# Performance work log

Measured on AMD Instinct MI355X. Metric: run time of the kernel, lower is better.

The kernel has to match this reference:

```python
import jax, jax.numpy as jnp
import numpy as np

N_NODES = 100000
N_EDGES = 1600000
IN_CH = 128
HID = 128
OUT_CH = 40


def setup_inputs() -> dict:
    key = jax.random.key(0)
    ks = jax.random.split(key, 8)
    x = jax.random.normal(ks[0], (N_NODES, IN_CH), dtype=jnp.float32)
    edge_index = jax.random.randint(ks[1], (2, N_EDGES), 0, N_NODES, dtype=jnp.int64)
    s1 = 1.0 / np.sqrt(IN_CH)
    s2 = 1.0 / np.sqrt(HID)
    # SAGEConv layer 1: lin_l (applied to aggregated neighbors, has bias), lin_r (applied to root, no bias)
    Wl1 = jax.random.uniform(ks[2], (IN_CH, HID), jnp.float32, -s1, s1)
    b1 = jnp.zeros((HID,), jnp.float32)
    Wr1 = jax.random.uniform(ks[3], (IN_CH, HID), jnp.float32, -s1, s1)
    # SAGEConv layer 2
    Wl2 = jax.random.uniform(ks[4], (HID, OUT_CH), jnp.float32, -s2, s2)
    b2 = jnp.zeros((OUT_CH,), jnp.float32)
    Wr2 = jax.random.uniform(ks[5], (HID, OUT_CH), jnp.float32, -s2, s2)
    return {"x": x, "edge_index": edge_index, "Wl1": Wl1, "b1": b1, "Wr1": Wr1,
            "Wl2": Wl2, "b2": b2, "Wr2": Wr2}


def _sage_conv(x, src, dst, Wl, b, Wr):
    # mean-aggregate source-node features onto target nodes (PyG SAGEConv, aggr='mean')
    msg_sum = jax.ops.segment_sum(x[src], dst, num_segments=N_NODES)  # [N, F]
    deg = jax.ops.segment_sum(jnp.ones((src.shape[0],), x.dtype), dst, num_segments=N_NODES)
    aggr = msg_sum / jnp.maximum(deg, 1.0)[:, None]
    return aggr @ Wl + b + x @ Wr


def reference(x, edge_index, Wl1, b1, Wr1, Wl2, b2, Wr2):
    src, dst = edge_index[0], edge_index[1]
    h = _sage_conv(x, src, dst, Wl1, b1, Wr1)
    h = jax.nn.relu(h)  # dropout is identity in eval mode
    h = _sage_conv(h, src, dst, Wl2, b2, Wr2)
    return jax.nn.log_softmax(h, axis=-1)
```

## Files before the change

### kernel.cpp

```cpp
#include <hip/hip_runtime.h>
#include <math.h>

#define NN 100000
#define NE 1600000
#define NBUK ((NN + 255) / 256)
#define CAP 5120
#define NBLK_A 500
#define EPB (NE / NBLK_A)
#define GPB (EPB / 4)
#define MT ((NN + 127) / 128)
#define MPAD ((size_t)MT * 128)

typedef __attribute__((ext_vector_type(8))) short short8;
typedef __attribute__((ext_vector_type(4))) float f32x4;
typedef __attribute__((ext_vector_type(4))) int i32x4;
typedef unsigned short ushort_t;
typedef unsigned int uint_t;

__device__ inline ushort_t f2bf(float f) {
    uint_t u = __builtin_bit_cast(uint_t, f);
    u += 0x7FFFu + ((u >> 16) & 1u);
    return (ushort_t)(u >> 16);
}
__device__ inline float bits2f(uint_t u) { return __builtin_bit_cast(float, u); }
__device__ inline float lo16(uint_t u) { return bits2f(u << 16); }
__device__ inline float hi16(uint_t u) { return bits2f(u & 0xFFFF0000u); }

__device__ inline void gload_lds16(const void* g, void* l) {
    __builtin_amdgcn_global_load_lds(
        (const __attribute__((address_space(1))) unsigned int*)g,
        (__attribute__((address_space(3))) unsigned int*)l, 16, 0, 0);
}

__global__ __launch_bounds__(256) void cvt_bf16(const float* __restrict__ x,
                                                ushort_t* __restrict__ xb) {
    const int total = NN * 128 / 8;
    const f32x4* src = (const f32x4*)x;
    for (int g = blockIdx.x * 256 + threadIdx.x; g < total; g += gridDim.x * 256) {
        f32x4 v0 = __builtin_nontemporal_load(src + (size_t)g * 2);
        f32x4 v1 = __builtin_nontemporal_load(src + (size_t)g * 2 + 1);
        i32x4 o;
        o[0] = ((uint_t)f2bf(v0[1]) << 16) | (uint_t)f2bf(v0[0]);
        o[1] = ((uint_t)f2bf(v0[3]) << 16) | (uint_t)f2bf(v0[2]);
        o[2] = ((uint_t)f2bf(v1[1]) << 16) | (uint_t)f2bf(v1[0]);
        o[3] = ((uint_t)f2bf(v1[3]) << 16) | (uint_t)f2bf(v1[2]);
        *(i32x4*)(xb + (size_t)g * 8) = o;
    }
}

__global__ void pack_weights(const float* __restrict__ Wl1, const float* __restrict__ Wr1,
                             const float* __restrict__ Wl2, const float* __restrict__ Wr2,
                             ushort_t* __restrict__ W1T, ushort_t* __restrict__ W2T) {
    int gid = blockIdx.x * blockDim.x + threadIdx.x;
    if (gid < 256 * 128) {
        int n = gid >> 7, k = gid & 127;
        float v = (n < 128) ? Wl1[k * 128 + n] : Wr1[k * 128 + (n - 128)];
        W1T[gid] = f2bf(v);
    } else {
        int g = gid - 256 * 128;
        if (g < 128 * 128) {
            int n = g >> 7, k = g & 127;
            float v = 0.0f;
            if (n < 40)      v = Wl2[k * 40 + n];
            else if (n < 80) v = Wr2[k * 40 + (n - 40)];
            W2T[g] = f2bf(v);
        }
    }
}

__global__ __launch_bounds__(256) void hist_buckets(const int* __restrict__ ei,
                                                    int* __restrict__ bhist) {
    __shared__ int h[NBUK];
    int tid = threadIdx.x;
    for (int i = tid; i < NBUK; i += 256) h[i] = 0;
    __syncthreads();
    const i32x4* dsts = (const i32x4*)(ei + NE + blockIdx.x * EPB);
    for (int g = tid; g < GPB; g += 256) {
        i32x4 d = __builtin_nontemporal_load(dsts + g);
#pragma unroll
        for (int j = 0; j < 4; ++j) atomicAdd(&h[d[j] >> 8], 1);
    }
    __syncthreads();
    for (int i = tid; i < NBUK; i += 256)
        if (h[i]) atomicAdd(&bhist[i], h[i]);
}

__global__ __launch_bounds__(512) void scan_buckets(const int* __restrict__ bhist,
                                                    int* __restrict__ boff,
                                                    int* __restrict__ gcur,
                                                    int* __restrict__ offsets) {
    __shared__ int part[512];
    int t = threadIdx.x;
    int v = (t < NBUK) ? bhist[t] : 0;
    part[t] = v;
    __syncthreads();
    for (int d = 1; d < 512; d <<= 1) {
        int tmp = (t >= d) ? part[t - d] : 0;
        __syncthreads();
        part[t] += tmp;
        __syncthreads();
    }
    if (t <= NBUK) {
        int excl = (t == 0) ? 0 : part[t - 1];
        boff[t] = excl;
        if (t < NBUK) gcur[t] = excl;
    }
    if (t == 0) offsets[NN] = NE;
}

__global__ __launch_bounds__(256) void bin_pass(const int* __restrict__ ei,
                                                int* __restrict__ gcur,
                                                int* __restrict__ pairs) {
    __shared__ int h[NBUK];
    __shared__ int base[NBUK];
    int tid = threadIdx.x;
    for (int i = tid; i < NBUK; i += 256) h[i] = 0;
    __syncthreads();
    int e0 = blockIdx.x * EPB;
    const i32x4* dsts = (const i32x4*)(ei + NE + e0);
    const i32x4* srcs = (const i32x4*)(ei + e0);
    for (int g = tid; g < GPB; g += 256) {
        i32x4 d = __builtin_nontemporal_load(dsts + g);
#pragma unroll
        for (int j = 0; j < 4; ++j) atomicAdd(&h[d[j] >> 8], 1);
    }
    __syncthreads();
    for (int i = tid; i < NBUK; i += 256) {
        int c = h[i];
        base[i] = c ? atomicAdd(&gcur[i], c) : 0;
        h[i] = 0;
    }
    __syncthreads();
    for (int g = tid; g < GPB; g += 256) {
        i32x4 d = __builtin_nontemporal_load(dsts + g);
        i32x4 s = __builtin_nontemporal_load(srcs + g);
#pragma unroll
        for (int j = 0; j < 4; ++j) {
            int buk = d[j] >> 8;
            int pos = base[buk] + atomicAdd(&h[buk], 1);
            pairs[pos] = (s[j] << 8) | (d[j] & 255);
        }
    }
}

__global__ __launch_bounds__(256) void sort_buckets(const int* __restrict__ boff,
                                                    const int* __restrict__ pairs,
                                                    int* __restrict__ offsets,
                                                    int* __restrict__ ssrc) {
    __shared__ int plds[CAP];
    __shared__ int slds[CAP];
    __shared__ int cnt[256];
    __shared__ int excl[256];
    int buk = blockIdx.x, tid = threadIdx.x;
    int bstart = boff[buk], bend = boff[buk + 1];
    int count = min(bend - bstart, CAP);
    int lo = buk << 8;
    cnt[tid] = 0;
    __syncthreads();
    for (int j = tid; j < count; j += 256) {
        int p = pairs[bstart + j];
        plds[j] = p;
        atomicAdd(&cnt[p & 255], 1);
    }
    __syncthreads();
    int c = cnt[tid];
    excl[tid] = c;
    __syncthreads();
    for (int d = 1; d < 256; d <<= 1) {
        int tmp = (tid >= d) ? excl[tid - d] : 0;
        __syncthreads();
        excl[tid] += tmp;
        __syncthreads();
    }
    int myExcl = excl[tid] - c;
    __syncthreads();
    excl[tid] = myExcl;
    cnt[tid] = 0;
    __syncthreads();
    for (int j = tid; j < count; j += 256) {
        int p = plds[j];
        int loc = p & 255;
        int pos = excl[loc] + atomicAdd(&cnt[loc], 1);
        slds[pos] = p >> 8;
    }
    __syncthreads();
    for (int j = tid; j < count; j += 256) ssrc[bstart + j] = slds[j];
    if (lo + tid < NN) offsets[lo + tid] = bstart + myExcl;
}

__global__ __launch_bounds__(256, 2) void gemm_mfma(const ushort_t* __restrict__ A,
                                                    const ushort_t* __restrict__ Bt,
                                                    ushort_t* __restrict__ G,
                                                    float* __restrict__ Croot,
                                                    int M, int split, int rootEnd, int gstride) {
    __shared__ __align__(16) char As[128 * 256];
    __shared__ __align__(16) char Bs[128 * 256];
    int tid = threadIdx.x;
    int lane = tid & 63, wid = tid >> 6;
    int quad = lane >> 4, l15 = lane & 15;
    int wm = (wid & 1) * 64, wn = (wid >> 1) * 64;
    int mBase = blockIdx.x * 128, nBase = blockIdx.y * 128;
    int rootW = rootEnd - split;

    const char* aT = (const char*)(A + (size_t)mBase * 128);
    const char* bT = (const char*)(Bt + (size_t)nBase * 128);
#pragma unroll
    for (int ii = 0; ii < 8; ++ii) {
        int rr = (wid * 8 + ii) * 4 + quad;
        int src = rr * 256 + ((l15 * 16) ^ ((rr & 7) << 4));
        int ldsb = (wid * 8 + ii) * 1024;
        gload_lds16(aT + src, As + ldsb);
        gload_lds16(bT + src, Bs + ldsb);
    }
    asm volatile("s_waitcnt vmcnt(0)" ::: "memory");
    __syncthreads();

    f32x4 acc[4][4];
#pragma unroll
    for (int i = 0; i < 4; ++i)
#pragma unroll
        for (int j = 0; j < 4; ++j) acc[i][j] = (f32x4){0.f, 0.f, 0.f, 0.f};

#pragma unroll
    for (int kk = 0; kk < 4; ++kk) {
        int kByte = kk * 64 + quad * 16;
        short8 af[4], bfr[4];
#pragma unroll
        for (int i = 0; i < 4; ++i) {
            int row = wm + i * 16 + l15;
            af[i] = *(const short8*)(As + row * 256 + (kByte ^ ((row & 7) << 4)));
        }
#pragma unroll
        for (int j = 0; j < 4; ++j) {
            int row = wn + j * 16 + l15;
            bfr[j] = *(const short8*)(Bs + row * 256 + (kByte ^ ((row & 7) << 4)));
        }
#pragma unroll
        for (int i = 0; i < 4; ++i)
#pragma unroll
            for (int j = 0; j < 4; ++j)
                acc[i][j] = __builtin_amdgcn_mfma_f32_16x16x32_bf16(af[i], bfr[j],
                                                                    acc[i][j], 0, 0, 0);
    }

#pragma unroll
    for (int i = 0; i < 4; ++i) {
#pragma unroll
        for (int r = 0; r < 4; ++r) {
            int m = mBase + wm + i * 16 + quad * 4 + r;
            if (m >= M) continue;
#pragma unroll
            for (int j = 0; j < 4; ++j) {
                int n = nBase + wn + j * 16 + l15;
                float v = acc[i][j][r];
                if (n < split) G[(size_t)m * gstride + n] = f2bf(v);
                else if (n < rootEnd) Croot[(size_t)m * rootW + (n - split)] = v;
            }
        }
    }
}

__global__ __launch_bounds__(256) void aggregate1(const int* __restrict__ offsets,
                                                  const int* __restrict__ ssrc,
                                                  const ushort_t* __restrict__ G1,
                                                  const float* __restrict__ C1root,
                                                  const float* __restrict__ b1,
                                                  ushort_t* __restrict__ s1b) {
    int w = (blockIdx.x * blockDim.x + threadIdx.x) >> 6;
    int lane = threadIdx.x & 63;
    if (w >= NN) return;
    int start = offsets[w], end = offsets[w + 1];
    int g = lane >> 4, q = lane & 15;
    const char* Gb = (const char*)G1;
    int qb = q << 4;
    float a0 = 0.f, a1 = 0.f, a2 = 0.f, a3 = 0.f, a4 = 0.f, a5 = 0.f, a6 = 0.f, a7 = 0.f;
    for (int base = start; base < end; base += 64) {
        int cnt = min(64, end - base);
        int idx = (base + lane < end) ? ssrc[base + lane] : 0;
        int j = 0;
        for (; j + 16 <= cnt; j += 16) {
            int s0 = __shfl(idx, j + g, 64);
            int s1 = __shfl(idx, j + 4 + g, 64);
            int s2 = __shfl(idx, j + 8 + g, 64);
            int s3 = __shfl(idx, j + 12 + g, 64);
            uint4 u0 = *(const uint4*)(Gb + (s0 << 8) + qb);
            uint4 u1 = *(const uint4*)(Gb + (s1 << 8) + qb);
            uint4 u2 = *(const uint4*)(Gb + (s2 << 8) + qb);
            uint4 u3 = *(const uint4*)(Gb + (s3 << 8) + qb);
            a0 += (lo16(u0.x) + lo16(u1.x)) + (lo16(u2.x) + lo16(u3.x));
            a1 += (hi16(u0.x) + hi16(u1.x)) + (hi16(u2.x) + hi16(u3.x));
            a2 += (lo16(u0.y) + lo16(u1.y)) + (lo16(u2.y) + lo16(u3.y));
            a3 += (hi16(u0.y) + hi16(u1.y)) + (hi16(u2.y) + hi16(u3.y));
            a4 += (lo16(u0.z) + lo16(u1.z)) + (lo16(u2.z) + lo16(u3.z));
            a5 += (hi16(u0.z) + hi16(u1.z)) + (hi16(u2.z) + hi16(u3.z));
            a6 += (lo16(u0.w) + lo16(u1.w)) + (lo16(u2.w) + lo16(u3.w));
            a7 += (hi16(u0.w) + hi16(u1.w)) + (hi16(u2.w) + hi16(u3.w));
        }
        for (; j + 8 <= cnt; j += 8) {
            int s0 = __shfl(idx, j + g, 64);
            int s1 = __shfl(idx, j + 4 + g, 64);
            uint4 u0 = *(const uint4*)(Gb + (s0 << 8) + qb);
            uint4 u1 = *(const uint4*)(Gb + (s1 << 8) + qb);
            a0 += lo16(u0.x) + lo16(u1.x);
            a1 += hi16(u0.x) + hi16(u1.x);
            a2 += lo16(u0.y) + lo16(u1.y);
            a3 += hi16(u0.y) + hi16(u1.y);
            a4 += lo16(u0.z) + lo16(u1.z);
            a5 += hi16(u0.z) + hi16(u1.z);
            a6 += lo16(u0.w) + lo16(u1.w);
            a7 += hi16(u0.w) + hi16(u1.w);
        }
        for (; j < cnt; j += 4) {
            int e = j + g;
            int s0 = __shfl(idx, (e < cnt) ? e : 0, 64);
            if (e < cnt) {
                uint4 u0 = *(const uint4*)(Gb + (s0 << 8) + qb);
                a0 += lo16(u0.x); a1 += hi16(u0.x);
                a2 += lo16(u0.y); a3 += hi16(u0.y);
                a4 += lo16(u0.z); a5 += hi16(u0.z);
                a6 += lo16(u0.w); a7 += hi16(u0.w);
            }
        }
    }
    a0 += __shfl_xor(a0, 16, 64); a0 += __shfl_xor(a0, 32, 64);
    a1 += __shfl_xor(a1, 16, 64); a1 += __shfl_xor(a1, 32, 64);
    a2 += __shfl_xor(a2, 16, 64); a2 += __shfl_xor(a2, 32, 64);
    a3 += __shfl_xor(a3, 16, 64); a3 += __shfl_xor(a3, 32, 64);
    a4 += __shfl_xor(a4, 16, 64); a4 += __shfl_xor(a4, 32, 64);
    a5 += __shfl_xor(a5, 16, 64); a5 += __shfl_xor(a5, 32, 64);
    a6 += __shfl_xor(a6, 16, 64); a6 += __shfl_xor(a6, 32, 64);
    a7 += __shfl_xor(a7, 16, 64); a7 += __shfl_xor(a7, 32, 64);
    if (g == 0) {
        float inv = 1.0f / fmaxf((float)(end - start), 1.0f);
        float4 r0 = *(const float4*)(C1root + (size_t)w * 128 + q * 8);
        float4 r1 = *(const float4*)(C1root + (size_t)w * 128 + q * 8 + 4);
        float4 c0 = *(const float4*)(b1 + q * 8);
        float4 c1 = *(const float4*)(b1 + q * 8 + 4);
        float h0 = fmaxf(a0 * inv + c0.x + r0.x, 0.f);
        float h1 = fmaxf(a1 * inv + c0.y + r0.y, 0.f);
        float h2 = fmaxf(a2 * inv + c0.z + r0.z, 0.f);
        float h3 = fmaxf(a3 * inv + c0.w + r0.w, 0.f);
        float h4 = fmaxf(a4 * inv + c1.x + r1.x, 0.f);
        float h5 = fmaxf(a5 * inv + c1.y + r1.y, 0.f);
        float h6 = fmaxf(a6 * inv + c1.z + r1.z, 0.f);
        float h7 = fmaxf(a7 * inv + c1.w + r1.w, 0.f);
        uint4 o;
        o.x = ((uint_t)f2bf(h1) << 16) | (uint_t)f2bf(h0);
        o.y = ((uint_t)f2bf(h3) << 16) | (uint_t)f2bf(h2);
        o.z = ((uint_t)f2bf(h5) << 16) | (uint_t)f2bf(h4);
        o.w = ((uint_t)f2bf(h7) << 16) | (uint_t)f2bf(h6);
        *(uint4*)((char*)s1b + (size_t)w * 256 + qb) = o;
    }
}

__global__ __launch_bounds__(256) void aggregate2(const int* __restrict__ offsets,
                                                  const int* __restrict__ ssrc,
                                                  const ushort_t* __restrict__ G2,
                                                  const float* __restrict__ C2root,
                                                  const float* __restrict__ b2,
                                                  float* __restrict__ out) {
    int w = (blockIdx.x * blockDim.x + threadIdx.x) >> 6;
    int lane = threadIdx.x & 63;
    if (w >= NN) return;
    int start = offsets[w], end = offsets[w + 1];
    int g = lane >> 4, q = lane & 15;
    bool act = q < 10;
    int qb = q << 3;
    const char* Gb = (const char*)G2;
    float a0 = 0.f, a1 = 0.f, a2 = 0.f, a3 = 0.f;
    for (int base = start; base < end; base += 64) {
        int cnt = min(64, end - base);
        int idx = (base + lane < end) ? ssrc[base + lane] : 0;
        int j = 0;
        for (; j + 16 <= cnt; j += 16) {
            int s0 = __shfl(idx, j + g, 64);
            int s1 = __shfl(idx, j + 4 + g, 64);
            int s2 = __shfl(idx, j + 8 + g, 64);
            int s3 = __shfl(idx, j + 12 + g, 64);
            if (act) {
                uint2 u0 = *(const uint2*)(Gb + (s0 << 7) + qb);
                uint2 u1 = *(const uint2*)(Gb + (s1 << 7) + qb);
                uint2 u2 = *(const uint2*)(Gb + (s2 << 7) + qb);
                uint2 u3 = *(const uint2*)(Gb + (s3 << 7) + qb);
                a0 += (lo16(u0.x) + lo16(u1.x)) + (lo16(u2.x) + lo16(u3.x));
                a1 += (hi16(u0.x) + hi16(u1.x)) + (hi16(u2.x) + hi16(u3.x));
                a2 += (lo16(u0.y) + lo16(u1.y)) + (lo16(u2.y) + lo16(u3.y));
                a3 += (hi16(u0.y) + hi16(u1.y)) + (hi16(u2.y) + hi16(u3.y));
            }
        }
        for (; j + 8 <= cnt; j += 8) {
            int s0 = __shfl(idx, j + g, 64);
            int s1 = __shfl(idx, j + 4 + g, 64);
            if (act) {
                uint2 u0 = *(const uint2*)(Gb + (s0 << 7) + qb);
                uint2 u1 = *(const uint2*)(Gb + (s1 << 7) + qb);
                a0 += lo16(u0.x) + lo16(u1.x);
                a1 += hi16(u0.x) + hi16(u1.x);
                a2 += lo16(u0.y) + lo16(u1.y);
                a3 += hi16(u0.y) + hi16(u1.y);
            }
        }
        for (; j < cnt; j += 4) {
            int e = j + g;
            int s0 = __shfl(idx, (e < cnt) ? e : 0, 64);
            if (act && e < cnt) {
                uint2 u0 = *(const uint2*)(Gb + (s0 << 7) + qb);
                a0 += lo16(u0.x); a1 += hi16(u0.x);
                a2 += lo16(u0.y); a3 += hi16(u0.y);
            }
        }
    }
    a0 += __shfl_xor(a0, 16, 64); a0 += __shfl_xor(a0, 32, 64);
    a1 += __shfl_xor(a1, 16, 64); a1 += __shfl_xor(a1, 32, 64);
    a2 += __shfl_xor(a2, 16, 64); a2 += __shfl_xor(a2, 32, 64);
    a3 += __shfl_xor(a3, 16, 64); a3 += __shfl_xor(a3, 32, 64);
    if (g == 0) {
        float inv = 1.0f / fmaxf((float)(end - start), 1.0f);
        float v0 = -INFINITY, v1 = -INFINITY, v2 = -INFINITY, v3 = -INFINITY;
        if (act) {
            float4 r = *(const float4*)(C2root + (size_t)w * 40 + q * 4);
            float4 bb = *(const float4*)(b2 + q * 4);
            v0 = a0 * inv + bb.x + r.x;
            v1 = a1 * inv + bb.y + r.y;
            v2 = a2 * inv + bb.z + r.z;
            v3 = a3 * inv + bb.w + r.w;
        }
        float m = fmaxf(fmaxf(v0, v1), fmaxf(v2, v3));
#pragma unroll
        for (int d = 8; d >= 1; d >>= 1) m = fmaxf(m, __shfl_xor(m, d, 64));
        float e = act ? (expf(v0 - m) + expf(v1 - m)) + (expf(v2 - m) + expf(v3 - m)) : 0.f;
#pragma unroll
        for (int d = 8; d >= 1; d >>= 1) e += __shfl_xor(e, d, 64);
        float lse = m + logf(e);
        if (act) {
            float4 o = make_float4(v0 - lse, v1 - lse, v2 - lse, v3 - lse);
            *(float4*)(out + (size_t)w * 40 + q * 4) = o;
        }
    }
}

extern "C" void kernel_launch(void* const* d_in, const int* in_sizes, int n_in,
                              void* d_out, int out_size, void* d_ws, size_t ws_size,
                              hipStream_t stream) {
    const float* x   = (const float*)d_in[0];
    const int*   ei  = (const int*)d_in[1];
    const float* Wl1 = (const float*)d_in[2];
    const float* b1  = (const float*)d_in[3];
    const float* Wr1 = (const float*)d_in[4];
    const float* Wl2 = (const float*)d_in[5];
    const float* b2  = (const float*)d_in[6];
    const float* Wr2 = (const float*)d_in[7];
    float* out = (float*)d_out;

    char* ws = (char*)d_ws;
    size_t off = 0;
    auto alloc = [&](size_t bytes) -> void* {
        void* p = ws + off;
        off = (off + bytes + 255) & ~(size_t)255;
        return p;
    };
    int*      bhist   = (int*)alloc((size_t)NBUK * 4);
    int*      boff    = (int*)alloc((size_t)(NBUK + 1) * 4);
    int*      gcur    = (int*)alloc((size_t)NBUK * 4);
    int*      pairs   = (int*)alloc((size_t)NE * 4);
    int*      offsets = (int*)alloc((size_t)(NN + 1) * 4);
    int*      ssrc    = (int*)alloc((size_t)NE * 4);
    ushort_t* W1T     = (ushort_t*)alloc((size_t)256 * 128 * 2);
    ushort_t* W2T     = (ushort_t*)alloc((size_t)128 * 128 * 2);
    ushort_t* xb      = (ushort_t*)alloc(MPAD * 128 * 2);
    ushort_t* G1      = (ushort_t*)alloc((size_t)NN * 128 * 2);
    float*    C1root  = (float*)alloc((size_t)NN * 128 * 4);
    ushort_t* s1b     = (ushort_t*)alloc(MPAD * 128 * 2);
    ushort_t* G2      = (ushort_t*)alloc((size_t)NN * 64 * 2);
    float*    C2root  = (float*)alloc((size_t)NN * 40 * 4);

    hipMemsetAsync(bhist, 0, (size_t)NBUK * 4, stream);

    cvt_bf16<<<2048, 256, 0, stream>>>(x, xb);
    pack_weights<<<192, 256, 0, stream>>>(Wl1, Wr1, Wl2, Wr2, W1T, W2T);
    hist_buckets<<<NBLK_A, 256, 0, stream>>>(ei, bhist);
    scan_buckets<<<1, 512, 0, stream>>>(bhist, boff, gcur, offsets);
    bin_pass<<<NBLK_A, 256, 0, stream>>>(ei, gcur, pairs);
    sort_buckets<<<NBUK, 256, 0, stream>>>(boff, pairs, offsets, ssrc);

    dim3 g1(MT, 2);
    gemm_mfma<<<g1, 256, 0, stream>>>(xb, W1T, G1, C1root, NN, 128, 256, 128);

    aggregate1<<<(NN * 64 + 255) / 256, 256, 0, stream>>>(offsets, ssrc, G1, C1root, b1, s1b);

    dim3 g2(MT, 1);
    gemm_mfma<<<g2, 256, 0, stream>>>(s1b, W2T, G2, C2root, NN, 40, 80, 64);

    aggregate2<<<(NN * 64 + 255) / 256, 256, 0, stream>>>(offsets, ssrc, G2, C2root, b2, out);
}
```

Before: 331.5 us.

## Fuse front-end kernels and store root projections and layer-2 messages compactly in bf16

```diff
diff --git a/kernel.cpp b/kernel.cpp
--- a/kernel.cpp
+++ b/kernel.cpp
@@ -10,6 +10,9 @@
 #define GPB (EPB / 4)
 #define MT ((NN + 127) / 128)
 #define MPAD ((size_t)MT * 128)
+#define PACK_B 192
+#define CVT_B0 (NBLK_A + PACK_B)
+#define FRONT_GRID 2048
 
 typedef __attribute__((ext_vector_type(8))) short short8;
 typedef __attribute__((ext_vector_type(4))) float f32x4;
@@ -32,57 +35,61 @@
         (__attribute__((address_space(3))) unsigned int*)l, 16, 0, 0);
 }
 
-__global__ __launch_bounds__(256) void cvt_bf16(const float* __restrict__ x,
-                                                ushort_t* __restrict__ xb) {
-    const int total = NN * 128 / 8;
-    const f32x4* src = (const f32x4*)x;
-    for (int g = blockIdx.x * 256 + threadIdx.x; g < total; g += gridDim.x * 256) {
-        f32x4 v0 = __builtin_nontemporal_load(src + (size_t)g * 2);
-        f32x4 v1 = __builtin_nontemporal_load(src + (size_t)g * 2 + 1);
-        i32x4 o;
-        o[0] = ((uint_t)f2bf(v0[1]) << 16) | (uint_t)f2bf(v0[0]);
-        o[1] = ((uint_t)f2bf(v0[3]) << 16) | (uint_t)f2bf(v0[2]);
-        o[2] = ((uint_t)f2bf(v1[1]) << 16) | (uint_t)f2bf(v1[0]);
-        o[3] = ((uint_t)f2bf(v1[3]) << 16) | (uint_t)f2bf(v1[2]);
-        *(i32x4*)(xb + (size_t)g * 8) = o;
-    }
-}
-
-__global__ void pack_weights(const float* __restrict__ Wl1, const float* __restrict__ Wr1,
-                             const float* __restrict__ Wl2, const float* __restrict__ Wr2,
-                             ushort_t* __restrict__ W1T, ushort_t* __restrict__ W2T) {
-    int gid = blockIdx.x * blockDim.x + threadIdx.x;
-    if (gid < 256 * 128) {
-        int n = gid >> 7, k = gid & 127;
-        float v = (n < 128) ? Wl1[k * 128 + n] : Wr1[k * 128 + (n - 128)];
-        W1T[gid] = f2bf(v);
+__global__ __launch_bounds__(256) void front(const float* __restrict__ x,
+                                             ushort_t* __restrict__ xb,
+                                             const float* __restrict__ Wl1,
+                                             const float* __restrict__ Wr1,
+                                             const float* __restrict__ Wl2,
+                                             const float* __restrict__ Wr2,
+                                             ushort_t* __restrict__ W1T,
+                                             ushort_t* __restrict__ W2T,
+                                             const int* __restrict__ ei,
+                                             int* __restrict__ bhist) {
+    __shared__ int h[NBUK];
+    int bid = blockIdx.x, tid = threadIdx.x;
+    if (bid < NBLK_A) {
+        for (int i = tid; i < NBUK; i += 256) h[i] = 0;
+        __syncthreads();
+        const i32x4* dsts = (const i32x4*)(ei + NE + bid * EPB);
+        for (int g = tid; g < GPB; g += 256) {
+            i32x4 d = __builtin_nontemporal_load(dsts + g);
+#pragma unroll
+            for (int j = 0; j < 4; ++j) atomicAdd(&h[d[j] >> 8], 1);
+        }
+        __syncthreads();
+        for (int i = tid; i < NBUK; i += 256)
+            if (h[i]) atomicAdd(&bhist[i], h[i]);
+    } else if (bid < CVT_B0) {
+        int gid = (bid - NBLK_A) * 256 + tid;
+        if (gid < 256 * 128) {
+            int n = gid >> 7, k = gid & 127;
+            float v = (n < 128) ? Wl1[k * 128 + n] : Wr1[k * 128 + (n - 128)];
+            W1T[gid] = f2bf(v);
+        } else {
+            int g = gid - 256 * 128;
+            if (g < 128 * 128) {
+                int n = g >> 7, k = g & 127;
+                float v = 0.0f;
+                if (n < 40)      v = Wl2[k * 40 + n];
+                else if (n < 80) v = Wr2[k * 40 + (n - 40)];
+                W2T[g] = f2bf(v);
+            }
+        }
     } else {
-        int g = gid - 256 * 128;
-        if (g < 128 * 128) {
-            int n = g >> 7, k = g & 127;
-            float v = 0.0f;
-            if (n < 40)      v = Wl2[k * 40 + n];
-            else if (n < 80) v = Wr2[k * 40 + (n - 40)];
-            W2T[g] = f2bf(v);
-        }
-    }
-}
-
-__global__ __launch_bounds__(256) void hist_buckets(const int* __restrict__ ei,
-                                                    int* __restrict__ bhist) {
-    __shared__ int h[NBUK];
-    int tid = threadIdx.x;
-    for (int i = tid; i < NBUK; i += 256) h[i] = 0;
-    __syncthreads();
-    const i32x4* dsts = (const i32x4*)(ei + NE + blockIdx.x * EPB);
-    for (int g = tid; g < GPB; g += 256) {
-        i32x4 d = __builtin_nontemporal_load(dsts + g);
-#pragma unroll
-        for (int j = 0; j < 4; ++j) atomicAdd(&h[d[j] >> 8], 1);
-    }
-    __syncthreads();
-    for (int i = tid; i < NBUK; i += 256)
-        if (h[i]) atomicAdd(&bhist[i], h[i]);
+        const int total = NN * 128 / 8;
+        const int nb = FRONT_GRID - CVT_B0;
+        const f32x4* src = (const f32x4*)x;
+        for (int g = (bid - CVT_B0) * 256 + tid; g < total; g += nb * 256) {
+            f32x4 v0 = __builtin_nontemporal_load(src + (size_t)g * 2);
+            f32x4 v1 = __builtin_nontemporal_load(src + (size_t)g * 2 + 1);
+            i32x4 o;
+            o[0] = ((uint_t)f2bf(v0[1]) << 16) | (uint_t)f2bf(v0[0]);
+            o[1] = ((uint_t)f2bf(v0[3]) << 16) | (uint_t)f2bf(v0[2]);
+            o[2] = ((uint_t)f2bf(v1[1]) << 16) | (uint_t)f2bf(v1[0]);
+            o[3] = ((uint_t)f2bf(v1[3]) << 16) | (uint_t)f2bf(v1[2]);
+            *(i32x4*)(xb + (size_t)g * 8) = o;
+        }
+    }
 }
 
 __global__ __launch_bounds__(512) void scan_buckets(const int* __restrict__ bhist,
@@ -191,7 +198,7 @@
 __global__ __launch_bounds__(256, 2) void gemm_mfma(const ushort_t* __restrict__ A,
                                                     const ushort_t* __restrict__ Bt,
                                                     ushort_t* __restrict__ G,
-                                                    float* __restrict__ Croot,
+                                                    ushort_t* __restrict__ Croot,
                                                     int M, int split, int rootEnd, int gstride) {
     __shared__ __align__(16) char As[128 * 256];
     __shared__ __align__(16) char Bs[128 * 256];
@@ -254,7 +261,7 @@
                 int n = nBase + wn + j * 16 + l15;
                 float v = acc[i][j][r];
                 if (n < split) G[(size_t)m * gstride + n] = f2bf(v);
-                else if (n < rootEnd) Croot[(size_t)m * rootW + (n - split)] = v;
+                else if (n < rootEnd) Croot[(size_t)m * rootW + (n - split)] = f2bf(v);
             }
         }
     }
@@ -263,7 +270,7 @@
 __global__ __launch_bounds__(256) void aggregate1(const int* __restrict__ offsets,
                                                   const int* __restrict__ ssrc,
                                                   const ushort_t* __restrict__ G1,
-                                                  const float* __restrict__ C1root,
+                                                  const ushort_t* __restrict__ C1root,
                                                   const float* __restrict__ b1,
                                                   ushort_t* __restrict__ s1b) {
     int w = (blockIdx.x * blockDim.x + threadIdx.x) >> 6;
@@ -332,18 +339,17 @@
     a7 += __shfl_xor(a7, 16, 64); a7 += __shfl_xor(a7, 32, 64);
     if (g == 0) {
         float inv = 1.0f / fmaxf((float)(end - start), 1.0f);
-        float4 r0 = *(const float4*)(C1root + (size_t)w * 128 + q * 8);
-        float4 r1 = *(const float4*)(C1root + (size_t)w * 128 + q * 8 + 4);
+        uint4 rv = *(const uint4*)((const char*)C1root + (size_t)w * 256 + qb);
         float4 c0 = *(const float4*)(b1 + q * 8);
         float4 c1 = *(const float4*)(b1 + q * 8 + 4);
-        float h0 = fmaxf(a0 * inv + c0.x + r0.x, 0.f);
-        float h1 = fmaxf(a1 * inv + c0.y + r0.y, 0.f);
-        float h2 = fmaxf(a2 * inv + c0.z + r0.z, 0.f);
-        float h3 = fmaxf(a3 * inv + c0.w + r0.w, 0.f);
-        float h4 = fmaxf(a4 * inv + c1.x + r1.x, 0.f);
-        float h5 = fmaxf(a5 * inv + c1.y + r1.y, 0.f);
-        float h6 = fmaxf(a6 * inv + c1.z + r1.z, 0.f);
-        float h7 = fmaxf(a7 * inv + c1.w + r1.w, 0.f);
+        float h0 = fmaxf(a0 * inv + c0.x + lo16(rv.x), 0.f);
+        float h1 = fmaxf(a1 * inv + c0.y + hi16(rv.x), 0.f);
+        float h2 = fmaxf(a2 * inv + c0.z + lo16(rv.y), 0.f);
+        float h3 = fmaxf(a3 * inv + c0.w + hi16(rv.y), 0.f);
+        float h4 = fmaxf(a4 * inv + c1.x + lo16(rv.z), 0.f);
+        float h5 = fmaxf(a5 * inv + c1.y + hi16(rv.z), 0.f);
+        float h6 = fmaxf(a6 * inv + c1.z + lo16(rv.w), 0.f);
+        float h7 = fmaxf(a7 * inv + c1.w + hi16(rv.w), 0.f);
         uint4 o;
         o.x = ((uint_t)f2bf(h1) << 16) | (uint_t)f2bf(h0);
         o.y = ((uint_t)f2bf(h3) << 16) | (uint_t)f2bf(h2);
@@ -356,7 +362,7 @@
 __global__ __launch_bounds__(256) void aggregate2(const int* __restrict__ offsets,
                                                   const int* __restrict__ ssrc,
                                                   const ushort_t* __restrict__ G2,
-                                                  const float* __restrict__ C2root,
+                                                  const ushort_t* __restrict__ C2root,
                                                   const float* __restrict__ b2,
                                                   float* __restrict__ out) {
     int w = (blockIdx.x * blockDim.x + threadIdx.x) >> 6;
@@ -378,10 +384,10 @@
             int s2 = __shfl(idx, j + 8 + g, 64);
             int s3 = __shfl(idx, j + 12 + g, 64);
             if (act) {
-                uint2 u0 = *(const uint2*)(Gb + (s0 << 7) + qb);
-                uint2 u1 = *(const uint2*)(Gb + (s1 << 7) + qb);
-                uint2 u2 = *(const uint2*)(Gb + (s2 << 7) + qb);
-                uint2 u3 = *(const uint2*)(Gb + (s3 << 7) + qb);
+                uint2 u0 = *(const uint2*)(Gb + (size_t)s0 * 80 + qb);
+                uint2 u1 = *(const uint2*)(Gb + (size_t)s1 * 80 + qb);
+                uint2 u2 = *(const uint2*)(Gb + (size_t)s2 * 80 + qb);
+                uint2 u3 = *(const uint2*)(Gb + (size_t)s3 * 80 + qb);
                 a0 += (lo16(u0.x) + lo16(u1.x)) + (lo16(u2.x) + lo16(u3.x));
                 a1 += (hi16(u0.x) + hi16(u1.x)) + (hi16(u2.x) + hi16(u3.x));
                 a2 += (lo16(u0.y) + lo16(u1.y)) + (lo16(u2.y) + lo16(u3.y));
@@ -392,8 +398,8 @@
             int s0 = __shfl(idx, j + g, 64);
             int s1 = __shfl(idx, j + 4 + g, 64);
             if (act) {
-                uint2 u0 = *(const uint2*)(Gb + (s0 << 7) + qb);
-                uint2 u1 = *(const uint2*)(Gb + (s1 << 7) + qb);
+                uint2 u0 = *(const uint2*)(Gb + (size_t)s0 * 80 + qb);
+                uint2 u1 = *(const uint2*)(Gb + (size_t)s1 * 80 + qb);
                 a0 += lo16(u0.x) + lo16(u1.x);
                 a1 += hi16(u0.x) + hi16(u1.x);
                 a2 += lo16(u0.y) + lo16(u1.y);
@@ -404,7 +410,7 @@
             int e = j + g;
             int s0 = __shfl(idx, (e < cnt) ? e : 0, 64);
             if (act && e < cnt) {
-                uint2 u0 = *(const uint2*)(Gb + (s0 << 7) + qb);
+                uint2 u0 = *(const uint2*)(Gb + (size_t)s0 * 80 + qb);
                 a0 += lo16(u0.x); a1 += hi16(u0.x);
                 a2 += lo16(u0.y); a3 += hi16(u0.y);
             }
@@ -418,12 +424,12 @@
         float inv = 1.0f / fmaxf((float)(end - start), 1.0f);
         float v0 = -INFINITY, v1 = -INFINITY, v2 = -INFINITY, v3 = -INFINITY;
         if (act) {
-            float4 r = *(const float4*)(C2root + (size_t)w * 40 + q * 4);
+            uint2 rv = *(const uint2*)((const char*)C2root + (size_t)w * 80 + qb);
             float4 bb = *(const float4*)(b2 + q * 4);
-            v0 = a0 * inv + bb.x + r.x;
-            v1 = a1 * inv + bb.y + r.y;
-            v2 = a2 * inv + bb.z + r.z;
-            v3 = a3 * inv + bb.w + r.w;
+            v0 = a0 * inv + bb.x + lo16(rv.x);
+            v1 = a1 * inv + bb.y + hi16(rv.x);
+            v2 = a2 * inv + bb.z + lo16(rv.y);
+            v3 = a3 * inv + bb.w + hi16(rv.y);
         }
         float m = fmaxf(fmaxf(v0, v1), fmaxf(v2, v3));
 #pragma unroll
@@ -469,16 +475,14 @@
     ushort_t* W2T     = (ushort_t*)alloc((size_t)128 * 128 * 2);
     ushort_t* xb      = (ushort_t*)alloc(MPAD * 128 * 2);
     ushort_t* G1      = (ushort_t*)alloc((size_t)NN * 128 * 2);
-    float*    C1root  = (float*)alloc((size_t)NN * 128 * 4);
+    ushort_t* C1root  = (ushort_t*)alloc((size_t)NN * 128 * 2);
     ushort_t* s1b     = (ushort_t*)alloc(MPAD * 128 * 2);
-    ushort_t* G2      = (ushort_t*)alloc((size_t)NN * 64 * 2);
-    float*    C2root  = (float*)alloc((size_t)NN * 40 * 4);
+    ushort_t* G2      = (ushort_t*)alloc((size_t)NN * 40 * 2);
+    ushort_t* C2root  = (ushort_t*)alloc((size_t)NN * 40 * 2);
 
     hipMemsetAsync(bhist, 0, (size_t)NBUK * 4, stream);
 
-    cvt_bf16<<<2048, 256, 0, stream>>>(x, xb);
-    pack_weights<<<192, 256, 0, stream>>>(Wl1, Wr1, Wl2, Wr2, W1T, W2T);
-    hist_buckets<<<NBLK_A, 256, 0, stream>>>(ei, bhist);
+    front<<<FRONT_GRID, 256, 0, stream>>>(x, xb, Wl1, Wr1, Wl2, Wr2, W1T, W2T, ei, bhist);
     scan_buckets<<<1, 512, 0, stream>>>(bhist, boff, gcur, offsets);
     bin_pass<<<NBLK_A, 256, 0, stream>>>(ei, gcur, pairs);
     sort_buckets<<<NBUK, 256, 0, stream>>>(boff, pairs, offsets, ssrc);
@@ -489,7 +493,7 @@
     aggregate1<<<(NN * 64 + 255) / 256, 256, 0, stream>>>(offsets, ssrc, G1, C1root, b1, s1b);
 
     dim3 g2(MT, 1);
-    gemm_mfma<<<g2, 256, 0, stream>>>(s1b, W2T, G2, C2root, NN, 40, 80, 64);
+    gemm_mfma<<<g2, 256, 0, stream>>>(s1b, W2T, G2, C2root, NN, 40, 80, 40);
 
     aggregate2<<<(NN * 64 + 255) / 256, 256, 0, stream>>>(offsets, ssrc, G2, C2root, b2, out);
 }
```

Result: no change. 331.2 us (-0.1%).
